# Kernel optimization log

Measured on AMD Instinct MI355X. Metric: run time of the kernel, lower is better.

## Reference

```python
import jax, jax.numpy as jnp
import numpy as np

B, L, C, H = 4, 2048, 512, 8
D = C // H  # head_dim = 64


def _rope_tables(L, D):
    inv_freq = 1.0 / (10000.0 ** (np.arange(0, D, 2, dtype=np.float32) / D))
    t = np.arange(L, dtype=np.float32)
    freqs = np.outer(t, inv_freq)                      # (L, D/2)
    emb = np.concatenate([freqs, freqs], axis=-1)      # (L, D)
    return jnp.asarray(np.cos(emb)), jnp.asarray(np.sin(emb))


def setup_inputs() -> dict:
    key = jax.random.key(0)
    k1, k2, k3 = jax.random.split(key, 3)
    cos, sin = _rope_tables(L, D)
    return {
        "x": jax.random.normal(k1, (B, L, C), dtype=jnp.float32),
        "qkv_w": jax.random.normal(k2, (3 * C, C), dtype=jnp.float32) * 0.02,
        "qkv_b": jnp.zeros((3 * C,), dtype=jnp.float32),
        "proj_w": jax.random.normal(k3, (C, C), dtype=jnp.float32) * 0.02,
        "proj_b": jnp.zeros((C,), dtype=jnp.float32),
        "cos": cos,
        "sin": sin,
    }


def _rotate_half(x):
    x1, x2 = jnp.split(x, 2, axis=-1)
    return jnp.concatenate([-x2, x1], axis=-1)


def _apply_rope(x, cos, sin):
    # x: (B, H, L, D); cos/sin: (L, D)
    return x * cos[None, None] + _rotate_half(x) * sin[None, None]


def reference(x, qkv_w, qkv_b, proj_w, proj_b, cos, sin):
    b, l, c = x.shape
    scale = 1.0 / jnp.sqrt(jnp.float32(D))
    qkv = x @ qkv_w.T + qkv_b                          # (B, L, 3C)
    qkv = qkv.reshape(b, l, 3, H, D).transpose(2, 0, 3, 1, 4)  # (3, B, H, L, D)
    q, k, v = qkv[0], qkv[1], qkv[2]
    q = _apply_rope(q, cos, sin)
    k = _apply_rope(k, cos, sin)
    attn = jax.nn.softmax(scale * jnp.einsum('bhqd,bhkd->bhqk', q, k), axis=-1)
    out = jnp.einsum('bhqk,bhkd->bhqd', attn, v)       # (B, H, L, D)
    out = out.transpose(0, 2, 1, 3).reshape(b, l, c)   # (B, L, C)
    return out @ proj_w.T + proj_b
```

## Files before the change

### kernel.cpp

```cpp
#include <hip/hip_runtime.h>

#define CDIM 512
#define LDIM 2048
#define BDIM 4
#define HDIM 8
#define DDIM 64

typedef __attribute__((ext_vector_type(8))) short bf16x8;
typedef __attribute__((ext_vector_type(4))) float f32x4;
typedef __attribute__((ext_vector_type(2))) float f32x2;
typedef __attribute__((ext_vector_type(8))) unsigned short ushort8;

static __device__ __forceinline__ unsigned short f2bf(float f) {
  unsigned u = __float_as_uint(f);
  return (unsigned short)((u + 0x7FFFu + ((u >> 16) & 1u)) >> 16);
}

__global__ __launch_bounds__(256) void convert_kernel(
    const float* __restrict__ x, const float* __restrict__ qw,
    const float* __restrict__ pw, unsigned short* __restrict__ xb,
    unsigned short* __restrict__ wb, unsigned short* __restrict__ pwb) {
  const size_t i = ((size_t)blockIdx.x * 256 + threadIdx.x) * 8;
  const float* src; unsigned short* dst; size_t off;
  if (i < 4194304) { src = x;  dst = xb;  off = i; }
  else if (i < 4980736) { src = qw; dst = wb;  off = i - 4194304; }
  else { src = pw; dst = pwb; off = i - 4980736; }
  const float4 a = *(const float4*)(src + off);
  const float4 b = *(const float4*)(src + off + 4);
  ushort8 h;
  h[0] = f2bf(a.x); h[1] = f2bf(a.y); h[2] = f2bf(a.z); h[3] = f2bf(a.w);
  h[4] = f2bf(b.x); h[5] = f2bf(b.y); h[6] = f2bf(b.z); h[7] = f2bf(b.w);
  *(ushort8*)(dst + off) = h;
}

__global__ __launch_bounds__(256) void qkv_gemm_kernel(
    const unsigned short* __restrict__ xb, const unsigned short* __restrict__ wb,
    const float* __restrict__ bias, const float* __restrict__ cosT,
    const float* __restrict__ sinT, unsigned short* __restrict__ qb,
    unsigned short* __restrict__ kb, unsigned short* __restrict__ vt) {
  __shared__ char As[16384];
  __shared__ char Bs[16384];
  const int t  = threadIdx.x;
  const int w  = t >> 6, lane = t & 63;
  const int lo = lane & 15, hi = lane >> 4;
  const int wm = w >> 1, wn = w & 1;
  const int flat = blockIdx.x;
  const int xcd = flat & 7, j = flat >> 3;
  const int m0 = (xcd + 8 * (j / 12)) * 128;
  const int n0 = (j % 12) * 128;

  f32x4 acc[4][4];
  #pragma unroll
  for (int mt = 0; mt < 4; ++mt)
    #pragma unroll
    for (int nt = 0; nt < 4; ++nt) acc[mt][nt] = (f32x4){0.f, 0.f, 0.f, 0.f};

  const int srow   = t >> 3;
  const int schunk = ((t & 7) ^ (srow & 7)) << 4;
  const char* Ag = (const char*)xb;
  const char* Bg = (const char*)wb;

  for (int kt = 0; kt < CDIM; kt += 64) {
    #pragma unroll
    for (int s = 0; s < 4; ++s) {
      const int r = s * 32 + srow;
      __builtin_amdgcn_global_load_lds(
          (const __attribute__((address_space(1))) unsigned int*)
              (Ag + (size_t)(m0 + r) * 1024 + kt * 2 + schunk),
          (__attribute__((address_space(3))) unsigned int*)(As + s * 4096 + w * 1024),
          16, 0, 0);
      __builtin_amdgcn_global_load_lds(
          (const __attribute__((address_space(1))) unsigned int*)
              (Bg + (size_t)(n0 + r) * 1024 + kt * 2 + schunk),
          (__attribute__((address_space(3))) unsigned int*)(Bs + s * 4096 + w * 1024),
          16, 0, 0);
    }
    __syncthreads();
    #pragma unroll
    for (int ks = 0; ks < 2; ++ks) {
      bf16x8 af[4], bfr[4];
      #pragma unroll
      for (int mt = 0; mt < 4; ++mt)
        af[mt] = *(const bf16x8*)(As + (wm * 64 + mt * 16 + lo) * 128
                                  + (((ks * 4 + hi) ^ (lo & 7)) << 4));
      #pragma unroll
      for (int nt = 0; nt < 4; ++nt)
        bfr[nt] = *(const bf16x8*)(Bs + (wn * 64 + nt * 16 + lo) * 128
                                   + (((ks * 4 + hi) ^ (lo & 7)) << 4));
      #pragma unroll
      for (int mt = 0; mt < 4; ++mt)
        #pragma unroll
        for (int nt = 0; nt < 4; ++nt)
          acc[mt][nt] = __builtin_amdgcn_mfma_f32_16x16x32_bf16(
              af[mt], bfr[nt], acc[mt][nt], 0, 0, 0);
    }
    __syncthreads();
  }

  const int nbase = n0 + wn * 64;
  const int typ   = nbase >> 9;
  const int hh    = (nbase >> 6) & 7;
  const int bb    = m0 >> 11;
  const int lbase = (m0 & 2047) + wm * 64;

  float bq[4];
  #pragma unroll
  for (int nt = 0; nt < 4; ++nt) bq[nt] = bias[nbase + nt * 16 + lo];
  #pragma unroll
  for (int mt = 0; mt < 4; ++mt)
    #pragma unroll
    for (int nt = 0; nt < 4; ++nt)
      #pragma unroll
      for (int reg = 0; reg < 4; ++reg) acc[mt][nt][reg] += bq[nt];

  if (typ == 2) {
    unsigned short* vbase = vt + (size_t)(bb * HDIM + hh) * DDIM * LDIM;
    #pragma unroll
    for (int mt = 0; mt < 4; ++mt)
      #pragma unroll
      for (int nt = 0; nt < 4; ++nt) {
        const int d = nt * 16 + lo;
        #pragma unroll
        for (int reg = 0; reg < 4; ++reg) {
          const int l = lbase + mt * 16 + hi * 4 + reg;
          vbase[(size_t)d * LDIM + l] = f2bf(acc[mt][nt][reg]);
        }
      }
  } else {
    unsigned short* dstb = (typ ? kb : qb) + (size_t)(bb * HDIM + hh) * LDIM * DDIM;
    #pragma unroll
    for (int mt = 0; mt < 4; ++mt)
      #pragma unroll
      for (int nt = 0; nt < 4; ++nt) {
        const int d   = nt * 16 + lo;
        const float sgn = (nt & 2) ? 1.f : -1.f;
        #pragma unroll
        for (int reg = 0; reg < 4; ++reg) {
          const int l = lbase + mt * 16 + hi * 4 + reg;
          const float c = cosT[l * 64 + d], s = sinT[l * 64 + d];
          const float v = acc[mt][nt][reg] * c + sgn * acc[mt][nt ^ 2][reg] * s;
          dstb[(size_t)l * DDIM + d] = f2bf(v);
        }
      }
  }
}

#define CLOG2 0.18033688f

__global__ __launch_bounds__(512, 4) void attn_kernel(
    unsigned short* __restrict__ qb, const unsigned short* __restrict__ kb,
    const unsigned short* __restrict__ vt) {
  __shared__ char Lds[65536];
  const int t    = threadIdx.x;
  const int w    = t >> 6, lane = t & 63;
  const int lo   = lane & 15, hi = lane >> 4;
  const int wq   = w & 3, half = w >> 2;
  const int flat = blockIdx.x;
  const int xcd  = flat & 7, jj = flat >> 3;
  const int bh   = xcd + 8 * (jj >> 4);
  const int q0   = (jj & 15) * 128 + wq * 32;
  const int kb0  = half * 1024;

  const char* Kb = (const char*)kb + (size_t)bh * (LDIM * DDIM * 2);
  const char* Vb = (const char*)vt + (size_t)bh * (LDIM * DDIM * 2);
  unsigned short* Qb = qb + (size_t)bh * (LDIM * DDIM);

  bf16x8 qf[2][2];
  #pragma unroll
  for (int g = 0; g < 2; ++g)
    #pragma unroll
    for (int kd = 0; kd < 2; ++kd)
      qf[g][kd] = *(const bf16x8*)((const char*)(Qb + (size_t)(q0 + g * 16 + lo) * DDIM)
                                   + kd * 64 + hi * 16);

  f32x4 o[2][4];
  float mrun[2] = {0.f, 0.f}, mc[2] = {0.f, 0.f}, lpart[2] = {0.f, 0.f};
  #pragma unroll
  for (int g = 0; g < 2; ++g)
    #pragma unroll
    for (int r = 0; r < 4; ++r) o[g][r] = (f32x4){0.f, 0.f, 0.f, 0.f};

  const int krow = wq * 8 + (lane >> 3);
  const int kch  = ((lane & 7) ^ (krow & 7)) << 4;
  const int vrow = wq * 16 + (lane >> 2);
  const int vch  = ((lane & 3) ^ ((vrow >> 1) & 3)) << 4;

  auto stage = [&](int tile, int buf) {
    __builtin_amdgcn_global_load_lds(
        (const __attribute__((address_space(1))) unsigned int*)
            (Kb + (size_t)(kb0 + tile * 32 + krow) * 128 + kch),
        (__attribute__((address_space(3))) unsigned int*)
            (Lds + (half * 2 + buf) * 4096 + wq * 1024),
        16, 0, 0);
    __builtin_amdgcn_global_load_lds(
        (const __attribute__((address_space(1))) unsigned int*)
            (Vb + (size_t)vrow * (LDIM * 2) + (size_t)(kb0 + tile * 32) * 2 + vch),
        (__attribute__((address_space(3))) unsigned int*)
            (Lds + 16384 + (half * 2 + buf) * 4096 + wq * 1024),
        16, 0, 0);
  };

  stage(0, 0);

  char* Pwb = Lds + 32768 + w * 4096;

  for (int kt = 0; kt < 32; ++kt) {
    const int cur = kt & 1;
    asm volatile("s_waitcnt vmcnt(0)");
    __builtin_amdgcn_s_barrier();
    __builtin_amdgcn_sched_barrier(0);
    const int nk = kt < 31 ? kt + 1 : 31;
    stage(nk, cur ^ 1);

    const char* Kl = Lds + (half * 2 + cur) * 4096;
    const char* Vl = Lds + 16384 + (half * 2 + cur) * 4096;

    f32x4 sv[2][2];
    __builtin_amdgcn_s_setprio(1);
    #pragma unroll
    for (int nt = 0; nt < 2; ++nt) {
      sv[0][nt] = (f32x4){0.f, 0.f, 0.f, 0.f};
      sv[1][nt] = (f32x4){0.f, 0.f, 0.f, 0.f};
      const int key = nt * 16 + lo;
      #pragma unroll
      for (int kd = 0; kd < 2; ++kd) {
        const bf16x8 kf = *(const bf16x8*)(Kl + key * 128
                            + (((kd * 4 + hi) ^ (key & 7)) << 4));
        sv[0][nt] = __builtin_amdgcn_mfma_f32_16x16x32_bf16(kf, qf[0][kd], sv[0][nt], 0, 0, 0);
        sv[1][nt] = __builtin_amdgcn_mfma_f32_16x16x32_bf16(kf, qf[1][kd], sv[1][nt], 0, 0, 0);
      }
    }
    __builtin_amdgcn_s_setprio(0);

    #pragma unroll
    for (int g = 0; g < 2; ++g) {
      const float* sflat = (const float*)sv[g];
      const f32x2 cc2 = {CLOG2, CLOG2};
      const f32x2 mm2 = {-mc[g], -mc[g]};
      float pv[8];
      float ps = 0.f;
      #pragma unroll
      for (int i = 0; i < 4; ++i) {
        f32x2 a; a[0] = sflat[2*i]; a[1] = sflat[2*i+1];
        f32x2 xr;
        asm("v_pk_fma_f32 %0, %1, %2, %3" : "=v"(xr) : "v"(a), "v"(cc2), "v"(mm2));
        float p0, p1;
        asm("v_exp_f32 %0, %1" : "=v"(p0) : "v"(xr[0]));
        asm("v_exp_f32 %0, %1" : "=v"(p1) : "v"(xr[1]));
        pv[2*i] = p0; pv[2*i+1] = p1;
        ps += p0; ps += p1;
      }

      if (__builtin_expect((bool)__ballot(ps > 65536.f), 0)) {
        float mx = -1e30f;
        #pragma unroll
        for (int i = 0; i < 8; ++i) mx = fmaxf(mx, sflat[i]);
        mx = fmaxf(mx, __shfl_xor(mx, 16));
        mx = fmaxf(mx, __shfl_xor(mx, 32));
        const float newm = fmaxf(mrun[g], mx);
        const float al   = exp2f((mrun[g] - newm) * CLOG2);
        lpart[g] *= al;
        #pragma unroll
        for (int r = 0; r < 4; ++r) {
          const float aq = __shfl(al, (hi << 2) + r);
          #pragma unroll
          for (int dt = 0; dt < 4; ++dt) o[g][dt][r] *= aq;
        }
        mrun[g] = newm;
        mc[g]   = newm * CLOG2;
        ps = 0.f;
        #pragma unroll
        for (int i = 0; i < 8; ++i) {
          const float p = exp2f(fmaf(sflat[i], CLOG2, -mc[g]));
          pv[i] = p;
          ps += p;
        }
      }
      lpart[g] += ps;

      #pragma unroll
      for (int nt = 0; nt < 2; ++nt) {
        unsigned w0, w1;
        asm("v_cvt_pk_bf16_f32 %0, %1, %2"
            : "=v"(w0) : "v"(pv[nt*4+0]), "v"(pv[nt*4+1]));
        asm("v_cvt_pk_bf16_f32 %0, %1, %2"
            : "=v"(w1) : "v"(pv[nt*4+2]), "v"(pv[nt*4+3]));
        uint2 d2; d2.x = w0; d2.y = w1;
        *(uint2*)(Pwb + g * 2048 + lo * 128
                  + ((nt * 32 + hi * 8) ^ ((lo & 7) << 4))) = d2;
      }
    }

    __builtin_amdgcn_s_setprio(1);
    {
      const bf16x8 pf0 = *(const bf16x8*)(Pwb + lo * 128
                           + ((hi ^ (lo & 7)) << 4));
      const bf16x8 pf1 = *(const bf16x8*)(Pwb + 2048 + lo * 128
                           + ((hi ^ (lo & 7)) << 4));
      #pragma unroll
      for (int dt = 0; dt < 4; ++dt) {
        const int d = dt * 16 + lo;
        const bf16x8 vf = *(const bf16x8*)(Vl + d * 64
                            + ((hi ^ ((d >> 1) & 3)) << 4));
        o[0][dt] = __builtin_amdgcn_mfma_f32_16x16x32_bf16(pf0, vf, o[0][dt], 0, 0, 0);
        o[1][dt] = __builtin_amdgcn_mfma_f32_16x16x32_bf16(pf1, vf, o[1][dt], 0, 0, 0);
      }
    }
    __builtin_amdgcn_s_setprio(0);

    __builtin_amdgcn_sched_barrier(0);
  }

  asm volatile("s_waitcnt vmcnt(0)");
  __syncthreads();

  float rs[2];
  #pragma unroll
  for (int g = 0; g < 2; ++g) {
    rs[g] = lpart[g];
    rs[g] += __shfl_xor(rs[g], 16);
    rs[g] += __shfl_xor(rs[g], 32);
  }

  if (half == 1) {
    #pragma unroll
    for (int g = 0; g < 2; ++g) {
      #pragma unroll
      for (int dt = 0; dt < 4; ++dt)
        #pragma unroll
        for (int r = 0; r < 4; ++r)
          *(float*)(Lds + wq * 8192
                    + ((g * 16 + hi * 4 + r) * 64 + dt * 16 + lo) * 4) = o[g][dt][r];
      if (hi == 0) {
        *(float*)(Lds + 32768 + wq * 256 + g * 64 + lo * 4)       = rs[g];
        *(float*)(Lds + 32768 + wq * 256 + 128 + g * 64 + lo * 4) = mrun[g];
      }
    }
  }
  __syncthreads();
  if (half == 0) {
    #pragma unroll
    for (int g = 0; g < 2; ++g)
      #pragma unroll
      for (int r = 0; r < 4; ++r) {
        const int qrow = hi * 4 + r;
        const float m_a = __shfl(mrun[g], qrow);
        const float l_a = __shfl(rs[g], qrow);
        const float l_b = *(const float*)(Lds + 32768 + wq * 256 + g * 64 + qrow * 4);
        const float m_b = *(const float*)(Lds + 32768 + wq * 256 + 128 + g * 64 + qrow * 4);
        const float m  = fmaxf(m_a, m_b);
        const float aa = exp2f((m_a - m) * CLOG2);
        const float ab = exp2f((m_b - m) * CLOG2);
        const float inv = 1.f / (l_a * aa + l_b * ab);
        const int q = q0 + g * 16 + qrow;
        #pragma unroll
        for (int dt = 0; dt < 4; ++dt) {
          const float ob = *(const float*)(Lds + wq * 8192
                            + ((g * 16 + qrow) * 64 + dt * 16 + lo) * 4);
          Qb[(size_t)q * DDIM + dt * 16 + lo] =
              f2bf((o[g][dt][r] * aa + ob * ab) * inv);
        }
      }
  }
}

__global__ __launch_bounds__(256) void proj_gemm_kernel(
    const unsigned short* __restrict__ ab, const unsigned short* __restrict__ pwb,
    const float* __restrict__ bias, float* __restrict__ out) {
  __shared__ char As[8192];
  __shared__ char Bs[16384];
  const int t  = threadIdx.x;
  const int w  = t >> 6, lane = t & 63;
  const int lo = lane & 15, hi = lane >> 4;
  const int wm = w >> 1, wn = w & 1;
  const int flat = blockIdx.x;
  const int xcd = flat & 7, j = flat >> 3;
  const int m0 = (xcd + 8 * (j >> 2)) * 64;
  const int n0 = (j & 3) * 128;

  f32x4 acc[2][4];
  #pragma unroll
  for (int mt = 0; mt < 2; ++mt)
    #pragma unroll
    for (int nt = 0; nt < 4; ++nt) acc[mt][nt] = (f32x4){0.f, 0.f, 0.f, 0.f};

  const int srow   = t >> 3;
  const int schunk = ((t & 7) ^ (srow & 7)) << 4;
  const char* Ag = (const char*)ab;
  const char* Bg = (const char*)pwb;

  for (int kt = 0; kt < CDIM; kt += 64) {
    const int hh = kt >> 6;
    #pragma unroll
    for (int s = 0; s < 2; ++s) {
      const int r = s * 32 + srow;
      const int m = m0 + r;
      const int bb = m >> 11, l = m & 2047;
      __builtin_amdgcn_global_load_lds(
          (const __attribute__((address_space(1))) unsigned int*)
              (Ag + ((size_t)(bb * HDIM + hh) * LDIM + l) * 128 + schunk),
          (__attribute__((address_space(3))) unsigned int*)(As + s * 4096 + w * 1024),
          16, 0, 0);
    }
    #pragma unroll
    for (int s = 0; s < 4; ++s) {
      const int r = s * 32 + srow;
      __builtin_amdgcn_global_load_lds(
          (const __attribute__((address_space(1))) unsigned int*)
              (Bg + (size_t)(n0 + r) * 1024 + kt * 2 + schunk),
          (__attribute__((address_space(3))) unsigned int*)(Bs + s * 4096 + w * 1024),
          16, 0, 0);
    }
    __syncthreads();
    #pragma unroll
    for (int ks = 0; ks < 2; ++ks) {
      bf16x8 af[2], bfr[4];
      #pragma unroll
      for (int mt = 0; mt < 2; ++mt)
        af[mt] = *(const bf16x8*)(As + (wm * 32 + mt * 16 + lo) * 128
                                  + (((ks * 4 + hi) ^ (lo & 7)) << 4));
      #pragma unroll
      for (int nt = 0; nt < 4; ++nt)
        bfr[nt] = *(const bf16x8*)(Bs + (wn * 64 + nt * 16 + lo) * 128
                                   + (((ks * 4 + hi) ^ (lo & 7)) << 4));
      #pragma unroll
      for (int mt = 0; mt < 2; ++mt)
        #pragma unroll
        for (int nt = 0; nt < 4; ++nt)
          acc[mt][nt] = __builtin_amdgcn_mfma_f32_16x16x32_bf16(
              af[mt], bfr[nt], acc[mt][nt], 0, 0, 0);
    }
    __syncthreads();
  }

  const int nn = n0 + wn * 64;
  float bp[4];
  #pragma unroll
  for (int nt = 0; nt < 4; ++nt) bp[nt] = bias[nn + nt * 16 + lo];
  #pragma unroll
  for (int mt = 0; mt < 2; ++mt)
    #pragma unroll
    for (int nt = 0; nt < 4; ++nt)
      #pragma unroll
      for (int reg = 0; reg < 4; ++reg) {
        const int m = m0 + wm * 32 + mt * 16 + hi * 4 + reg;
        out[(size_t)m * CDIM + nn + nt * 16 + lo] = acc[mt][nt][reg] + bp[nt];
      }
}

extern "C" void kernel_launch(void* const* d_in, const int* in_sizes, int n_in,
                              void* d_out, int out_size, void* d_ws, size_t ws_size,
                              hipStream_t stream) {
  const float* x      = (const float*)d_in[0];
  const float* qkv_w  = (const float*)d_in[1];
  const float* qkv_b  = (const float*)d_in[2];
  const float* proj_w = (const float*)d_in[3];
  const float* proj_b = (const float*)d_in[4];
  const float* cosT   = (const float*)d_in[5];
  const float* sinT   = (const float*)d_in[6];
  float* out = (float*)d_out;

  unsigned short* qb  = (unsigned short*)d_ws;
  unsigned short* kb  = qb + (size_t)BDIM * HDIM * LDIM * DDIM;
  unsigned short* vt  = kb + (size_t)BDIM * HDIM * LDIM * DDIM;
  unsigned short* xb  = vt + (size_t)BDIM * HDIM * LDIM * DDIM;
  unsigned short* wb  = xb + (size_t)BDIM * LDIM * CDIM;
  unsigned short* pwb = wb + (size_t)3 * CDIM * CDIM;

  convert_kernel<<<dim3(2560), 256, 0, stream>>>(x, qkv_w, proj_w, xb, wb, pwb);
  qkv_gemm_kernel<<<dim3(768), 256, 0, stream>>>(xb, wb, qkv_b, cosT, sinT,
                                                 qb, kb, vt);
  attn_kernel<<<dim3(512), 512, 0, stream>>>(qb, kb, vt);
  proj_gemm_kernel<<<dim3(512), 256, 0, stream>>>(qb, pwb, proj_b, out);
}
```

Before: 92.14 us.

## Load K/V fragments directly from global memory instead of staging through LDS

The attention kernel stops double-buffering K and V tiles in LDS through global_load_lds and instead has each wave read its MFMA K and V fragments straight from global memory (relying on L2/cache). The block shrinks from 512 to 256 threads with twice as many blocks, and LDS drops to about 16.5KB, so more blocks can be resident. This removes the per-iteration barriers and LDS round-trip. In exchange each wave issues redundant, less coalesced global loads with no explicit prefetch, so latency may be exposed.

```diff
diff --git a/kernel.cpp b/kernel.cpp
--- a/kernel.cpp
+++ b/kernel.cpp
@@ -147,18 +147,18 @@
 
 #define CLOG2 0.18033688f
 
-__global__ __launch_bounds__(512, 4) void attn_kernel(
+__global__ __launch_bounds__(256, 5) void attn_kernel(
     unsigned short* __restrict__ qb, const unsigned short* __restrict__ kb,
     const unsigned short* __restrict__ vt) {
-  __shared__ char Lds[65536];
+  __shared__ char Lds[16896];
   const int t    = threadIdx.x;
   const int w    = t >> 6, lane = t & 63;
   const int lo   = lane & 15, hi = lane >> 4;
-  const int wq   = w & 3, half = w >> 2;
+  const int wq   = w & 1, half = w >> 1;
   const int flat = blockIdx.x;
   const int xcd  = flat & 7, jj = flat >> 3;
-  const int bh   = xcd + 8 * (jj >> 4);
-  const int q0   = (jj & 15) * 128 + wq * 32;
+  const int bh   = xcd + 8 * (jj >> 5);
+  const int q0   = (jj & 31) * 64 + wq * 32;
   const int kb0  = half * 1024;
 
   const char* Kb = (const char*)kb + (size_t)bh * (LDIM * DDIM * 2);
@@ -180,40 +180,10 @@
     #pragma unroll
     for (int r = 0; r < 4; ++r) o[g][r] = (f32x4){0.f, 0.f, 0.f, 0.f};
 
-  const int krow = wq * 8 + (lane >> 3);
-  const int kch  = ((lane & 7) ^ (krow & 7)) << 4;
-  const int vrow = wq * 16 + (lane >> 2);
-  const int vch  = ((lane & 3) ^ ((vrow >> 1) & 3)) << 4;
-
-  auto stage = [&](int tile, int buf) {
-    __builtin_amdgcn_global_load_lds(
-        (const __attribute__((address_space(1))) unsigned int*)
-            (Kb + (size_t)(kb0 + tile * 32 + krow) * 128 + kch),
-        (__attribute__((address_space(3))) unsigned int*)
-            (Lds + (half * 2 + buf) * 4096 + wq * 1024),
-        16, 0, 0);
-    __builtin_amdgcn_global_load_lds(
-        (const __attribute__((address_space(1))) unsigned int*)
-            (Vb + (size_t)vrow * (LDIM * 2) + (size_t)(kb0 + tile * 32) * 2 + vch),
-        (__attribute__((address_space(3))) unsigned int*)
-            (Lds + 16384 + (half * 2 + buf) * 4096 + wq * 1024),
-        16, 0, 0);
-  };
-
-  stage(0, 0);
-
-  char* Pwb = Lds + 32768 + w * 4096;
+  char* Pwb = Lds + w * 4096;
 
   for (int kt = 0; kt < 32; ++kt) {
-    const int cur = kt & 1;
-    asm volatile("s_waitcnt vmcnt(0)");
-    __builtin_amdgcn_s_barrier();
-    __builtin_amdgcn_sched_barrier(0);
-    const int nk = kt < 31 ? kt + 1 : 31;
-    stage(nk, cur ^ 1);
-
-    const char* Kl = Lds + (half * 2 + cur) * 4096;
-    const char* Vl = Lds + 16384 + (half * 2 + cur) * 4096;
+    const int kbase = kb0 + kt * 32;
 
     f32x4 sv[2][2];
     __builtin_amdgcn_s_setprio(1);
@@ -221,16 +191,23 @@
     for (int nt = 0; nt < 2; ++nt) {
       sv[0][nt] = (f32x4){0.f, 0.f, 0.f, 0.f};
       sv[1][nt] = (f32x4){0.f, 0.f, 0.f, 0.f};
-      const int key = nt * 16 + lo;
+      const int key = kbase + nt * 16 + lo;
       #pragma unroll
       for (int kd = 0; kd < 2; ++kd) {
-        const bf16x8 kf = *(const bf16x8*)(Kl + key * 128
-                            + (((kd * 4 + hi) ^ (key & 7)) << 4));
+        const bf16x8 kf = *(const bf16x8*)(Kb + (size_t)key * 128 + (kd * 4 + hi) * 16);
         sv[0][nt] = __builtin_amdgcn_mfma_f32_16x16x32_bf16(kf, qf[0][kd], sv[0][nt], 0, 0, 0);
         sv[1][nt] = __builtin_amdgcn_mfma_f32_16x16x32_bf16(kf, qf[1][kd], sv[1][nt], 0, 0, 0);
       }
     }
     __builtin_amdgcn_s_setprio(0);
+
+    bf16x8 vf[4];
+    #pragma unroll
+    for (int dt = 0; dt < 4; ++dt) {
+      const int d = dt * 16 + lo;
+      vf[dt] = *(const bf16x8*)(Vb + (size_t)d * (LDIM * 2)
+                                + (size_t)(kbase + hi * 8) * 2);
+    }
 
     #pragma unroll
     for (int g = 0; g < 2; ++g) {
@@ -299,19 +276,13 @@
                            + ((hi ^ (lo & 7)) << 4));
       #pragma unroll
       for (int dt = 0; dt < 4; ++dt) {
-        const int d = dt * 16 + lo;
-        const bf16x8 vf = *(const bf16x8*)(Vl + d * 64
-                            + ((hi ^ ((d >> 1) & 3)) << 4));
-        o[0][dt] = __builtin_amdgcn_mfma_f32_16x16x32_bf16(pf0, vf, o[0][dt], 0, 0, 0);
-        o[1][dt] = __builtin_amdgcn_mfma_f32_16x16x32_bf16(pf1, vf, o[1][dt], 0, 0, 0);
+        o[0][dt] = __builtin_amdgcn_mfma_f32_16x16x32_bf16(pf0, vf[dt], o[0][dt], 0, 0, 0);
+        o[1][dt] = __builtin_amdgcn_mfma_f32_16x16x32_bf16(pf1, vf[dt], o[1][dt], 0, 0, 0);
       }
     }
     __builtin_amdgcn_s_setprio(0);
-
-    __builtin_amdgcn_sched_barrier(0);
-  }
-
-  asm volatile("s_waitcnt vmcnt(0)");
+  }
+
   __syncthreads();
 
   float rs[2];
@@ -332,8 +303,8 @@
           *(float*)(Lds + wq * 8192
                     + ((g * 16 + hi * 4 + r) * 64 + dt * 16 + lo) * 4) = o[g][dt][r];
       if (hi == 0) {
-        *(float*)(Lds + 32768 + wq * 256 + g * 64 + lo * 4)       = rs[g];
-        *(float*)(Lds + 32768 + wq * 256 + 128 + g * 64 + lo * 4) = mrun[g];
+        *(float*)(Lds + 16384 + wq * 256 + g * 64 + lo * 4)       = rs[g];
+        *(float*)(Lds + 16384 + wq * 256 + 128 + g * 64 + lo * 4) = mrun[g];
       }
     }
   }
@@ -346,8 +317,8 @@
         const int qrow = hi * 4 + r;
         const float m_a = __shfl(mrun[g], qrow);
         const float l_a = __shfl(rs[g], qrow);
-        const float l_b = *(const float*)(Lds + 32768 + wq * 256 + g * 64 + qrow * 4);
-        const float m_b = *(const float*)(Lds + 32768 + wq * 256 + 128 + g * 64 + qrow * 4);
+        const float l_b = *(const float*)(Lds + 16384 + wq * 256 + g * 64 + qrow * 4);
+        const float m_b = *(const float*)(Lds + 16384 + wq * 256 + 128 + g * 64 + qrow * 4);
         const float m  = fmaxf(m_a, m_b);
         const float aa = exp2f((m_a - m) * CLOG2);
         const float ab = exp2f((m_b - m) * CLOG2);
@@ -470,6 +441,6 @@
   convert_kernel<<<dim3(2560), 256, 0, stream>>>(x, qkv_w, proj_w, xb, wb, pwb);
   qkv_gemm_kernel<<<dim3(768), 256, 0, stream>>>(xb, wb, qkv_b, cosT, sinT,
                                                  qb, kb, vt);
-  attn_kernel<<<dim3(512), 512, 0, stream>>>(qb, kb, vt);
+  attn_kernel<<<dim3(1024), 256, 0, stream>>>(qb, kb, vt);
   proj_gemm_kernel<<<dim3(512), 256, 0, stream>>>(qb, pwb, proj_b, out);
 }
```

After: 184.0 us. 2x slower.

## Double-buffer LDS tiles in QKV and projection GEMMs to overlap loads with MFMA

Applied to the files above, without the earlier changes.

Both GEMM kernels get two LDS buffers per operand. The next K-tile is issued via global_load_lds while the current tile feeds the MFMAs, and one waitcnt-plus-barrier per iteration replaces the two __syncthreads. This hides global-load latency behind compute. The cost is doubled LDS use per block, which may lower occupancy, and the sync now rests on manual waitcnt and sched_barrier placement.

```diff
diff --git a/kernel.cpp b/kernel.cpp
--- a/kernel.cpp
+++ b/kernel.cpp
@@ -38,8 +38,8 @@
     const float* __restrict__ bias, const float* __restrict__ cosT,
     const float* __restrict__ sinT, unsigned short* __restrict__ qb,
     unsigned short* __restrict__ kb, unsigned short* __restrict__ vt) {
-  __shared__ char As[16384];
-  __shared__ char Bs[16384];
+  __shared__ char As[32768];
+  __shared__ char Bs[32768];
   const int t  = threadIdx.x;
   const int w  = t >> 6, lane = t & 63;
   const int lo = lane & 15, hi = lane >> 4;
@@ -60,32 +60,46 @@
   const char* Ag = (const char*)xb;
   const char* Bg = (const char*)wb;
 
-  for (int kt = 0; kt < CDIM; kt += 64) {
+  auto stage = [&](int kt, int buf) {
     #pragma unroll
     for (int s = 0; s < 4; ++s) {
       const int r = s * 32 + srow;
       __builtin_amdgcn_global_load_lds(
           (const __attribute__((address_space(1))) unsigned int*)
-              (Ag + (size_t)(m0 + r) * 1024 + kt * 2 + schunk),
-          (__attribute__((address_space(3))) unsigned int*)(As + s * 4096 + w * 1024),
+              (Ag + (size_t)(m0 + r) * 1024 + kt * 128 + schunk),
+          (__attribute__((address_space(3))) unsigned int*)
+              (As + buf * 16384 + s * 4096 + w * 1024),
           16, 0, 0);
       __builtin_amdgcn_global_load_lds(
           (const __attribute__((address_space(1))) unsigned int*)
-              (Bg + (size_t)(n0 + r) * 1024 + kt * 2 + schunk),
-          (__attribute__((address_space(3))) unsigned int*)(Bs + s * 4096 + w * 1024),
+              (Bg + (size_t)(n0 + r) * 1024 + kt * 128 + schunk),
+          (__attribute__((address_space(3))) unsigned int*)
+              (Bs + buf * 16384 + s * 4096 + w * 1024),
           16, 0, 0);
     }
-    __syncthreads();
+  };
+
+  stage(0, 0);
+
+  for (int kt = 0; kt < 8; ++kt) {
+    const int cur = kt & 1;
+    asm volatile("s_waitcnt vmcnt(0)");
+    __builtin_amdgcn_s_barrier();
+    __builtin_amdgcn_sched_barrier(0);
+    if (kt < 7) stage(kt + 1, cur ^ 1);
+
+    const char* Al = As + cur * 16384;
+    const char* Bl = Bs + cur * 16384;
     #pragma unroll
     for (int ks = 0; ks < 2; ++ks) {
       bf16x8 af[4], bfr[4];
       #pragma unroll
       for (int mt = 0; mt < 4; ++mt)
-        af[mt] = *(const bf16x8*)(As + (wm * 64 + mt * 16 + lo) * 128
+        af[mt] = *(const bf16x8*)(Al + (wm * 64 + mt * 16 + lo) * 128
                                   + (((ks * 4 + hi) ^ (lo & 7)) << 4));
       #pragma unroll
       for (int nt = 0; nt < 4; ++nt)
-        bfr[nt] = *(const bf16x8*)(Bs + (wn * 64 + nt * 16 + lo) * 128
+        bfr[nt] = *(const bf16x8*)(Bl + (wn * 64 + nt * 16 + lo) * 128
                                    + (((ks * 4 + hi) ^ (lo & 7)) << 4));
       #pragma unroll
       for (int mt = 0; mt < 4; ++mt)
@@ -94,7 +108,7 @@
           acc[mt][nt] = __builtin_amdgcn_mfma_f32_16x16x32_bf16(
               af[mt], bfr[nt], acc[mt][nt], 0, 0, 0);
     }
-    __syncthreads();
+    __builtin_amdgcn_sched_barrier(0);
   }
 
   const int nbase = n0 + wn * 64;
@@ -367,8 +381,8 @@
 __global__ __launch_bounds__(256) void proj_gemm_kernel(
     const unsigned short* __restrict__ ab, const unsigned short* __restrict__ pwb,
     const float* __restrict__ bias, float* __restrict__ out) {
-  __shared__ char As[8192];
-  __shared__ char Bs[16384];
+  __shared__ char As[16384];
+  __shared__ char Bs[32768];
   const int t  = threadIdx.x;
   const int w  = t >> 6, lane = t & 63;
   const int lo = lane & 15, hi = lane >> 4;
@@ -389,8 +403,8 @@
   const char* Ag = (const char*)ab;
   const char* Bg = (const char*)pwb;
 
-  for (int kt = 0; kt < CDIM; kt += 64) {
-    const int hh = kt >> 6;
+  auto stage = [&](int kt, int buf) {
+    const int hh = kt;
     #pragma unroll
     for (int s = 0; s < 2; ++s) {
       const int r = s * 32 + srow;
@@ -399,7 +413,8 @@
       __builtin_amdgcn_global_load_lds(
           (const __attribute__((address_space(1))) unsigned int*)
               (Ag + ((size_t)(bb * HDIM + hh) * LDIM + l) * 128 + schunk),
-          (__attribute__((address_space(3))) unsigned int*)(As + s * 4096 + w * 1024),
+          (__attribute__((address_space(3))) unsigned int*)
+              (As + buf * 8192 + s * 4096 + w * 1024),
           16, 0, 0);
     }
     #pragma unroll
@@ -407,21 +422,34 @@
       const int r = s * 32 + srow;
       __builtin_amdgcn_global_load_lds(
           (const __attribute__((address_space(1))) unsigned int*)
-              (Bg + (size_t)(n0 + r) * 1024 + kt * 2 + schunk),
-          (__attribute__((address_space(3))) unsigned int*)(Bs + s * 4096 + w * 1024),
+              (Bg + (size_t)(n0 + r) * 1024 + kt * 128 + schunk),
+          (__attribute__((address_space(3))) unsigned int*)
+              (Bs + buf * 16384 + s * 4096 + w * 1024),
           16, 0, 0);
     }
-    __syncthreads();
+  };
+
+  stage(0, 0);
+
+  for (int kt = 0; kt < 8; ++kt) {
+    const int cur = kt & 1;
+    asm volatile("s_waitcnt vmcnt(0)");
+    __builtin_amdgcn_s_barrier();
+    __builtin_amdgcn_sched_barrier(0);
+    if (kt < 7) stage(kt + 1, cur ^ 1);
+
+    const char* Al = As + cur * 8192;
+    const char* Bl = Bs + cur * 16384;
     #pragma unroll
     for (int ks = 0; ks < 2; ++ks) {
       bf16x8 af[2], bfr[4];
       #pragma unroll
       for (int mt = 0; mt < 2; ++mt)
-        af[mt] = *(const bf16x8*)(As + (wm * 32 + mt * 16 + lo) * 128
+        af[mt] = *(const bf16x8*)(Al + (wm * 32 + mt * 16 + lo) * 128
                                   + (((ks * 4 + hi) ^ (lo & 7)) << 4));
       #pragma unroll
       for (int nt = 0; nt < 4; ++nt)
-        bfr[nt] = *(const bf16x8*)(Bs + (wn * 64 + nt * 16 + lo) * 128
+        bfr[nt] = *(const bf16x8*)(Bl + (wn * 64 + nt * 16 + lo) * 128
                                    + (((ks * 4 + hi) ^ (lo & 7)) << 4));
       #pragma unroll
       for (int mt = 0; mt < 2; ++mt)
@@ -430,7 +458,7 @@
           acc[mt][nt] = __builtin_amdgcn_mfma_f32_16x16x32_bf16(
               af[mt], bfr[nt], acc[mt][nt], 0, 0, 0);
     }
-    __syncthreads();
+    __builtin_amdgcn_sched_barrier(0);
   }
 
   const int nn = n0 + wn * 64;
```

Result: no change. 91.05 us, median of 3 (-1.2%).
